# Kernel tuning notes

Measured on AMD Instinct MI355X. Metric: run time of the kernel, lower is better.

The kernel has to match this reference:

```python
import jax, jax.numpy as jnp
import numpy as np

N_NODES = 50000
N_EDGES = 800000
D_IN, D_HID, D_OUT = 128, 128, 256
EPS = 1e-12  # F.normalize eps


def _mean_aggr(h, src, dst, n):
    # scatter-mean of source features onto destination nodes
    msg_sum = jax.ops.segment_sum(h[src], dst, num_segments=n)
    deg = jax.ops.segment_sum(jnp.ones((src.shape[0],), h.dtype), dst, num_segments=n)
    return msg_sum / jnp.maximum(deg, 1.0)[:, None]


def _l2_normalize(h):
    # F.normalize(p=2, dim=1): divide by clamped L2 norm
    nrm = jnp.sqrt(jnp.sum(h * h, axis=1, keepdims=True))
    return h / jnp.maximum(nrm, EPS)


def setup_inputs() -> dict:
    key = jax.random.key(0)
    ks = jax.random.split(key, 8)
    x = jax.random.normal(ks[0], (N_NODES, D_IN), dtype=jnp.float32)
    edge_index = jax.random.randint(ks[1], (2, N_EDGES), 0, N_NODES, dtype=jnp.int64 if jax.config.read('jax_enable_x64') else jnp.int32)
    s = 1.0 / np.sqrt(D_IN)
    W1_l = jax.random.uniform(ks[2], (D_IN, D_HID), jnp.float32, -s, s)
    W1_r = jax.random.uniform(ks[3], (D_IN, D_HID), jnp.float32, -s, s)
    b1 = jnp.zeros((D_HID,), jnp.float32)
    s2 = 1.0 / np.sqrt(D_HID)
    W2_l = jax.random.uniform(ks[4], (D_HID, D_OUT), jnp.float32, -s2, s2)
    W2_r = jax.random.uniform(ks[5], (D_HID, D_OUT), jnp.float32, -s2, s2)
    b2 = jnp.zeros((D_OUT,), jnp.float32)
    return {"x": x, "edge_index": edge_index, "W1_l": W1_l, "W1_r": W1_r,
            "b1": b1, "W2_l": W2_l, "W2_r": W2_r, "b2": b2}


def reference(x, edge_index, W1_l, W1_r, b1, W2_l, W2_r, b2):
    src, dst = edge_index[0], edge_index[1]
    n = x.shape[0]
    # SAGEConv 1: lin_l(mean_aggr(x)) + lin_r(x) + bias
    h = _mean_aggr(x, src, dst, n) @ W1_l + x @ W1_r + b1
    # dropout is identity in eval mode
    h = _l2_normalize(jax.nn.sigmoid(h))
    # SAGEConv 2
    h = _mean_aggr(h, src, dst, n) @ W2_l + h @ W2_r + b2
    h = _l2_normalize(jax.nn.sigmoid(h))
    return jax.nn.log_softmax(h, axis=-1)
```

## Files before the change

### kernel.cpp

```cpp
#include <hip/hip_runtime.h>

#define NN 50000
#define NE 800000
#define NB 782
#define CAP 1536


__device__ __forceinline__ unsigned short f2bf(float f) {
    union { float f; unsigned u; } v; v.f = f;
    unsigned u = v.u;
    return (unsigned short)((u + 0x7fffu + ((u >> 16) & 1u)) >> 16);
}
__device__ __forceinline__ float bfu_lo(unsigned p) {
    union { unsigned u; float f; } v; v.u = p << 16; return v.f;
}
__device__ __forceinline__ float bfu_hi(unsigned p) {
    union { unsigned u; float f; } v; v.u = p & 0xffff0000u; return v.f;
}

typedef __bf16 bf16x8 __attribute__((ext_vector_type(8)));
typedef float f32x4 __attribute__((ext_vector_type(4)));
typedef unsigned uint4v __attribute__((ext_vector_type(4)));
union U16 { uint4 u; bf16x8 v; };
union U16v { uint4v q; bf16x8 v; };


__global__ __launch_bounds__(512) void binscatter_kernel(const int* __restrict__ src,
                                                         const int* __restrict__ dst,
                                                         int* __restrict__ bcnt,
                                                         unsigned* __restrict__ ebuf) {
    __shared__ int hist[NB];
    __shared__ int base[NB];
    const int BE = 8192;
    int tid = threadIdx.x;
    int e0 = blockIdx.x * BE;
    for (int i = tid; i < NB; i += 512) hist[i] = 0;
    __syncthreads();
    for (int i = tid; i < BE; i += 512) {
        int e = e0 + i;
        if (e < NE) atomicAdd(&hist[dst[e] >> 6], 1);
    }
    __syncthreads();
    for (int i = tid; i < NB; i += 512) {
        int c = hist[i];
        base[i] = c ? atomicAdd(&bcnt[i], c) : 0;
        hist[i] = 0;
    }
    __syncthreads();
    for (int i = tid; i < BE; i += 512) {
        int e = e0 + i;
        if (e < NE) {
            int d = dst[e], b = d >> 6;
            int slot = base[b] + atomicAdd(&hist[b], 1);
            if (slot < CAP)
                ebuf[(size_t)b * CAP + slot] = (unsigned)src[e] | ((unsigned)(d & 63) << 16);
        }
    }
}

__global__ __launch_bounds__(256) void csr_kernel(const int* __restrict__ bcnt,
                                                  const unsigned* __restrict__ ebuf,
                                                  int* __restrict__ rowptr,
                                                  int* __restrict__ col) {
    __shared__ int red[256];
    __shared__ int deg[64];
    __shared__ int cur[64];
    __shared__ int cbase_s;
    int b = blockIdx.x, tid = threadIdx.x;
    int s = 0;
    for (int i = tid; i < b; i += 256) s += bcnt[i];
    red[tid] = s;
    if (tid < 64) deg[tid] = 0;
    __syncthreads();
    for (int off = 128; off; off >>= 1) {
        if (tid < off) red[tid] += red[tid + off];
        __syncthreads();
    }
    if (tid == 0) cbase_s = red[0];
    __syncthreads();
    int cnt = bcnt[b], cbase = cbase_s;
    if (cnt > CAP) cnt = CAP;
    const unsigned* eb = ebuf + (size_t)b * CAP;
    for (int i = tid; i < cnt; i += 256) atomicAdd(&deg[(eb[i] >> 16) & 63], 1);
    __syncthreads();
    if (tid == 0) {
        int run = 0;
        for (int j = 0; j < 64; j++) { cur[j] = run; run += deg[j]; }
    }
    __syncthreads();
    int node = b * 64 + tid;
    if (tid < 64 && node < NN) rowptr[node] = cbase + cur[tid];
    if (b == NB - 1 && tid == 0) rowptr[NN] = NE;
    __syncthreads();
    for (int i = tid; i < cnt; i += 256) {
        unsigned e = eb[i];
        int pos = atomicAdd(&cur[(e >> 16) & 63], 1);
        col[cbase + pos] = (int)(e & 0xffffu);
    }
}


template <int N>
__device__ __forceinline__ void pack_one(const float* __restrict__ Wl,
                                         const float* __restrict__ Wr,
                                         unsigned short* __restrict__ Wp, int t) {
    int lane = t & 63, c = t >> 6;
    int ks = c & 7, nt = c >> 3;
    int n = nt * 16 + (lane & 15);
    int kq = ks * 32 + (lane >> 4) * 8;
    unsigned short tmp[8];
#pragma unroll
    for (int j = 0; j < 8; j++) {
        int k = kq + j;
        float w = (k < 128) ? Wl[(size_t)k * N + n] : Wr[(size_t)(k - 128) * N + n];
        tmp[j] = f2bf(w);
    }
    ((ushort4*)Wp)[(size_t)c * 128 + lane * 2 + 0] = make_ushort4(tmp[0], tmp[1], tmp[2], tmp[3]);
    ((ushort4*)Wp)[(size_t)c * 128 + lane * 2 + 1] = make_ushort4(tmp[4], tmp[5], tmp[6], tmp[7]);
}

#define CAST_BLK (NN * 128 / 4 / 256)

__global__ void castpack_kernel(const float* __restrict__ in, unsigned short* __restrict__ outp,
                                const float* __restrict__ W1l, const float* __restrict__ W1r,
                                unsigned short* __restrict__ W1p,
                                const float* __restrict__ W2l, const float* __restrict__ W2r,
                                unsigned short* __restrict__ W2p) {
    if (blockIdx.x < CAST_BLK) {
        int i = blockIdx.x * 256 + threadIdx.x;
        float4 f = ((const float4*)in)[i];
        ushort4 o;
        o.x = f2bf(f.x); o.y = f2bf(f.y); o.z = f2bf(f.z); o.w = f2bf(f.w);
        ((ushort4*)outp)[i] = o;
    } else {
        int t = (blockIdx.x - CAST_BLK) * 256 + threadIdx.x;
        if (t < 8 * 8 * 64) pack_one<128>(W1l, W1r, W1p, t);
        else if (t < 8 * 8 * 64 + 16 * 8 * 64) pack_one<256>(W2l, W2r, W2p, t - 8 * 8 * 64);
    }
}


__global__ void aggregate_bf_kernel(const int* __restrict__ rowptr, const int* __restrict__ col,
                                    const uint4* __restrict__ feat4,
                                    uint4* __restrict__ out4) {
    int wid = (blockIdx.x * blockDim.x + threadIdx.x) >> 6;
    int lane = threadIdx.x & 63;
    if (wid >= NN) return;
    int beg = rowptr[wid], end = rowptr[wid + 1];
    int deg = end - beg;
    int g = lane >> 4, c16 = lane & 15;
    int nmain = deg < 64 ? deg : 64;
    int cidx = (lane < nmain) ? col[beg + lane] : 0;
    float acc[8];
#pragma unroll
    for (int j = 0; j < 8; j++) acc[j] = 0.f;
    for (int i = 0; i < nmain; i += 16) {
        int e0 = i + g, e1 = i + 4 + g, e2 = i + 8 + g, e3 = i + 12 + g;
        int s0 = __shfl(cidx, e0);
        int s1 = __shfl(cidx, e1);
        int s2 = __shfl(cidx, e2);
        int s3 = __shfl(cidx, e3);
        uint4 v0 = make_uint4(0u, 0u, 0u, 0u);
        uint4 v1 = make_uint4(0u, 0u, 0u, 0u);
        uint4 v2 = make_uint4(0u, 0u, 0u, 0u);
        uint4 v3 = make_uint4(0u, 0u, 0u, 0u);
        if (e0 < nmain) v0 = feat4[(size_t)s0 * 16 + c16];
        if (e1 < nmain) v1 = feat4[(size_t)s1 * 16 + c16];
        if (e2 < nmain) v2 = feat4[(size_t)s2 * 16 + c16];
        if (e3 < nmain) v3 = feat4[(size_t)s3 * 16 + c16];
        acc[0] += bfu_lo(v0.x); acc[1] += bfu_hi(v0.x);
        acc[2] += bfu_lo(v0.y); acc[3] += bfu_hi(v0.y);
        acc[4] += bfu_lo(v0.z); acc[5] += bfu_hi(v0.z);
        acc[6] += bfu_lo(v0.w); acc[7] += bfu_hi(v0.w);
        acc[0] += bfu_lo(v1.x); acc[1] += bfu_hi(v1.x);
        acc[2] += bfu_lo(v1.y); acc[3] += bfu_hi(v1.y);
        acc[4] += bfu_lo(v1.z); acc[5] += bfu_hi(v1.z);
        acc[6] += bfu_lo(v1.w); acc[7] += bfu_hi(v1.w);
        acc[0] += bfu_lo(v2.x); acc[1] += bfu_hi(v2.x);
        acc[2] += bfu_lo(v2.y); acc[3] += bfu_hi(v2.y);
        acc[4] += bfu_lo(v2.z); acc[5] += bfu_hi(v2.z);
        acc[6] += bfu_lo(v2.w); acc[7] += bfu_hi(v2.w);
        acc[0] += bfu_lo(v3.x); acc[1] += bfu_hi(v3.x);
        acc[2] += bfu_lo(v3.y); acc[3] += bfu_hi(v3.y);
        acc[4] += bfu_lo(v3.z); acc[5] += bfu_hi(v3.z);
        acc[6] += bfu_lo(v3.w); acc[7] += bfu_hi(v3.w);
    }
    for (int i = 64; i < deg; i += 4) {
        int idx = beg + i + g;
        if (idx < end) {
            int s = col[idx];
            uint4 v = feat4[(size_t)s * 16 + c16];
            acc[0] += bfu_lo(v.x); acc[1] += bfu_hi(v.x);
            acc[2] += bfu_lo(v.y); acc[3] += bfu_hi(v.y);
            acc[4] += bfu_lo(v.z); acc[5] += bfu_hi(v.z);
            acc[6] += bfu_lo(v.w); acc[7] += bfu_hi(v.w);
        }
    }
#pragma unroll
    for (int j = 0; j < 8; j++) {
        acc[j] += __shfl_xor(acc[j], 16);
        acc[j] += __shfl_xor(acc[j], 32);
    }
    if (g == 0) {
        float inv = (deg > 0) ? 1.0f / (float)deg : 0.0f;
        uint4 o;
        o.x = (unsigned)f2bf(acc[0] * inv) | ((unsigned)f2bf(acc[1] * inv) << 16);
        o.y = (unsigned)f2bf(acc[2] * inv) | ((unsigned)f2bf(acc[3] * inv) << 16);
        o.z = (unsigned)f2bf(acc[4] * inv) | ((unsigned)f2bf(acc[5] * inv) << 16);
        o.w = (unsigned)f2bf(acc[6] * inv) | ((unsigned)f2bf(acc[7] * inv) << 16);
        out4[(size_t)wid * 16 + c16] = o;
    }
}


template <int N, bool FINAL>
__global__ __launch_bounds__(512, 2) void gemm_mfma_kernel(
    const unsigned short* __restrict__ A0, const unsigned short* __restrict__ A1,
    const unsigned short* __restrict__ Wp, const float* __restrict__ bias,
    void* __restrict__ outp, int M) {
    const int NT = N / 32;
    __shared__ float redS[2][64];
    __shared__ float redE[2][64];
    int tid = threadIdx.x, wave = tid >> 6, lane = tid & 63;
    int half = wave & 1;
    int rg = wave >> 1;
    int quad = lane >> 4, col = lane & 15;
    int m_base = blockIdx.x * 64 + rg * 16;
    int row = m_base + col;
    int row_ld = row < M ? row : M - 1;

    bf16x8 a[8];
    const uint4* a0p = (const uint4*)(A0 + (size_t)row_ld * 128 + quad * 8);
    const uint4* a1p = (const uint4*)(A1 + (size_t)row_ld * 128 + quad * 8);
#pragma unroll
    for (int ks = 0; ks < 4; ks++) { U16 u; u.u = a0p[ks * 4]; a[ks] = u.v; }
#pragma unroll
    for (int ks = 0; ks < 4; ks++) { U16 u; u.u = a1p[ks * 4]; a[4 + ks] = u.v; }

    f32x4 acc[NT];
#pragma unroll
    for (int nt = 0; nt < NT; nt++) acc[nt] = (f32x4){0.f, 0.f, 0.f, 0.f};

    const uint4* wp = (const uint4*)Wp;
#pragma unroll
    for (int ks = 0; ks < 8; ks++) {
        uint4v w[NT];
#pragma unroll
        for (int j = 0; j < NT; j++) {
            const uint4* ap = wp + ((size_t)((half * NT + j) * 8 + ks) * 64 + lane);
            asm volatile("global_load_dwordx4 %0, %1, off" : "=&v"(w[j]) : "v"(ap));
        }
        asm volatile("s_waitcnt vmcnt(0)" ::: "memory");
        __builtin_amdgcn_sched_barrier(0);
#pragma unroll
        for (int j = 0; j < NT; j++) {
            U16v u; u.q = w[j];
            acc[j] = __builtin_amdgcn_mfma_f32_16x16x32_bf16(a[ks], u.v, acc[j], 0, 0, 0);
        }
    }

    int rbase = rg * 16 + quad * 4;

    float ssq[4] = {0.f, 0.f, 0.f, 0.f};
#pragma unroll
    for (int nt = 0; nt < NT; nt++) {
        float bv = bias[half * (NT * 16) + nt * 16 + col];
#pragma unroll
        for (int r = 0; r < 4; r++) {
            float z = acc[nt][r] + bv;
            float s = 1.0f / (1.0f + __expf(-z));
            acc[nt][r] = s;
            ssq[r] += s * s;
        }
    }
#pragma unroll
    for (int r = 0; r < 4; r++) {
#pragma unroll
        for (int off = 1; off < 16; off <<= 1) ssq[r] += __shfl_xor(ssq[r], off, 16);
    }
    if (col == 0) {
#pragma unroll
        for (int r = 0; r < 4; r++) redS[half][rbase + r] = ssq[r];
    }
    __syncthreads();
#pragma unroll
    for (int r = 0; r < 4; r++) {
        float tot = redS[0][rbase + r] + redS[1][rbase + r];
        float sc = 1.0f / fmaxf(sqrtf(tot), 1e-12f);
#pragma unroll
        for (int nt = 0; nt < NT; nt++) acc[nt][r] *= sc;
    }

    if (FINAL) {
        float se[4];
#pragma unroll
        for (int r = 0; r < 4; r++) {
            se[r] = 0.f;
#pragma unroll
            for (int nt = 0; nt < NT; nt++) se[r] += __expf(acc[nt][r]);
#pragma unroll
            for (int off = 1; off < 16; off <<= 1) se[r] += __shfl_xor(se[r], off, 16);
        }
        if (col == 0) {
#pragma unroll
            for (int r = 0; r < 4; r++) redE[half][rbase + r] = se[r];
        }
        __syncthreads();
        float* op = (float*)outp;
#pragma unroll
        for (int r = 0; r < 4; r++) {
            float lse = __logf(redE[0][rbase + r] + redE[1][rbase + r]);
            int m = m_base + quad * 4 + r;
            if (m < M) {
#pragma unroll
                for (int nt = 0; nt < NT; nt++)
                    op[(size_t)m * N + half * (NT * 16) + nt * 16 + col] = acc[nt][r] - lse;
            }
        }
    } else {
        unsigned short* op = (unsigned short*)outp;
#pragma unroll
        for (int r = 0; r < 4; r++) {
            int m = m_base + quad * 4 + r;
            if (m < M) {
#pragma unroll
                for (int nt = 0; nt < NT; nt++)
                    op[(size_t)m * N + half * (NT * 16) + nt * 16 + col] = f2bf(acc[nt][r]);
            }
        }
    }
}


extern "C" void kernel_launch(void* const* d_in, const int* in_sizes, int n_in,
                              void* d_out, int out_size, void* d_ws, size_t ws_size,
                              hipStream_t stream) {
    const float* x   = (const float*)d_in[0];
    const int*   ei  = (const int*)d_in[1];
    const float* W1l = (const float*)d_in[2];
    const float* W1r = (const float*)d_in[3];
    const float* b1  = (const float*)d_in[4];
    const float* W2l = (const float*)d_in[5];
    const float* W2r = (const float*)d_in[6];
    const float* b2  = (const float*)d_in[7];
    float* out = (float*)d_out;

    const int* src = ei;
    const int* dst = ei + NE;

    char* ws = (char*)d_ws;
    size_t off = 0;
    auto alloc = [&](size_t bytes) -> void* {
        void* p = ws + off;
        off += (bytes + 255) / 256 * 256;
        return p;
    };
    int* rowptr     = (int*)alloc((size_t)(NN + 1) * 4);
    int* col        = (int*)alloc((size_t)NE * 4);
    int* bcnt       = (int*)alloc((size_t)NB * 4);
    unsigned* ebuf  = (unsigned*)alloc((size_t)NB * CAP * 4);
    unsigned short* x_bf   = (unsigned short*)alloc((size_t)NN * 128 * 2);
    unsigned short* agg_bf = (unsigned short*)alloc((size_t)NN * 128 * 2);
    unsigned short* h1_bf  = (unsigned short*)alloc((size_t)NN * 128 * 2);
    unsigned short* W1p    = (unsigned short*)alloc((size_t)8 * 8 * 64 * 8 * 2);
    unsigned short* W2p    = (unsigned short*)alloc((size_t)16 * 8 * 64 * 8 * 2);

    hipMemsetAsync(bcnt, 0, (size_t)NB * 4, stream);
    binscatter_kernel<<<(NE + 8191) / 8192, 512, 0, stream>>>(src, dst, bcnt, ebuf);
    csr_kernel<<<NB, 256, 0, stream>>>(bcnt, ebuf, rowptr, col);

    castpack_kernel<<<CAST_BLK + 48, 256, 0, stream>>>(x, x_bf, W1l, W1r, W1p, W2l, W2r, W2p);

    aggregate_bf_kernel<<<(NN + 3) / 4, 256, 0, stream>>>(rowptr, col, (const uint4*)x_bf,
                                                          (uint4*)agg_bf);
    gemm_mfma_kernel<128, false><<<(NN + 63) / 64, 512, 0, stream>>>(agg_bf, x_bf, W1p, b1,
                                                                     h1_bf, NN);
    aggregate_bf_kernel<<<(NN + 3) / 4, 256, 0, stream>>>(rowptr, col, (const uint4*)h1_bf,
                                                          (uint4*)agg_bf);
    gemm_mfma_kernel<256, true><<<(NN + 63) / 64, 512, 0, stream>>>(agg_bf, h1_bf, W2p, b2,
                                                                    out, NN);
}
```

Before: 232.1 us.

## Fuse neighbor mean aggregation into the MFMA layer GEMM kernel via shared memory

The separate aggregation kernel is merged into the GEMM kernel. Each 512-thread block first gathers and averages neighbor features for its 64 rows into a padded LDS tile, then runs the MFMA GEMM reading the aggregated operand from LDS. This removes the agg_bf global write and re-read plus two kernel launches per forward pass. In exchange, the gather phase runs with only the GEMM kernel's occupancy (launch bounds 512,2), each wave walks 8 nodes serially, and a block barrier is added, which may hide gather latency less well than the standalone aggregation kernel did.

After: 242.3 us. 4.4% more time.

```diff
diff --git a/kernel.cpp b/kernel.cpp
--- a/kernel.cpp
+++ b/kernel.cpp
@@ -140,100 +140,103 @@
 }
 
 
-__global__ void aggregate_bf_kernel(const int* __restrict__ rowptr, const int* __restrict__ col,
-                                    const uint4* __restrict__ feat4,
-                                    uint4* __restrict__ out4) {
-    int wid = (blockIdx.x * blockDim.x + threadIdx.x) >> 6;
-    int lane = threadIdx.x & 63;
-    if (wid >= NN) return;
-    int beg = rowptr[wid], end = rowptr[wid + 1];
-    int deg = end - beg;
-    int g = lane >> 4, c16 = lane & 15;
-    int nmain = deg < 64 ? deg : 64;
-    int cidx = (lane < nmain) ? col[beg + lane] : 0;
-    float acc[8];
-#pragma unroll
-    for (int j = 0; j < 8; j++) acc[j] = 0.f;
-    for (int i = 0; i < nmain; i += 16) {
-        int e0 = i + g, e1 = i + 4 + g, e2 = i + 8 + g, e3 = i + 12 + g;
-        int s0 = __shfl(cidx, e0);
-        int s1 = __shfl(cidx, e1);
-        int s2 = __shfl(cidx, e2);
-        int s3 = __shfl(cidx, e3);
-        uint4 v0 = make_uint4(0u, 0u, 0u, 0u);
-        uint4 v1 = make_uint4(0u, 0u, 0u, 0u);
-        uint4 v2 = make_uint4(0u, 0u, 0u, 0u);
-        uint4 v3 = make_uint4(0u, 0u, 0u, 0u);
-        if (e0 < nmain) v0 = feat4[(size_t)s0 * 16 + c16];
-        if (e1 < nmain) v1 = feat4[(size_t)s1 * 16 + c16];
-        if (e2 < nmain) v2 = feat4[(size_t)s2 * 16 + c16];
-        if (e3 < nmain) v3 = feat4[(size_t)s3 * 16 + c16];
-        acc[0] += bfu_lo(v0.x); acc[1] += bfu_hi(v0.x);
-        acc[2] += bfu_lo(v0.y); acc[3] += bfu_hi(v0.y);
-        acc[4] += bfu_lo(v0.z); acc[5] += bfu_hi(v0.z);
-        acc[6] += bfu_lo(v0.w); acc[7] += bfu_hi(v0.w);
-        acc[0] += bfu_lo(v1.x); acc[1] += bfu_hi(v1.x);
-        acc[2] += bfu_lo(v1.y); acc[3] += bfu_hi(v1.y);
-        acc[4] += bfu_lo(v1.z); acc[5] += bfu_hi(v1.z);
-        acc[6] += bfu_lo(v1.w); acc[7] += bfu_hi(v1.w);
-        acc[0] += bfu_lo(v2.x); acc[1] += bfu_hi(v2.x);
-        acc[2] += bfu_lo(v2.y); acc[3] += bfu_hi(v2.y);
-        acc[4] += bfu_lo(v2.z); acc[5] += bfu_hi(v2.z);
-        acc[6] += bfu_lo(v2.w); acc[7] += bfu_hi(v2.w);
-        acc[0] += bfu_lo(v3.x); acc[1] += bfu_hi(v3.x);
-        acc[2] += bfu_lo(v3.y); acc[3] += bfu_hi(v3.y);
-        acc[4] += bfu_lo(v3.z); acc[5] += bfu_hi(v3.z);
-        acc[6] += bfu_lo(v3.w); acc[7] += bfu_hi(v3.w);
-    }
-    for (int i = 64; i < deg; i += 4) {
-        int idx = beg + i + g;
-        if (idx < end) {
-            int s = col[idx];
-            uint4 v = feat4[(size_t)s * 16 + c16];
-            acc[0] += bfu_lo(v.x); acc[1] += bfu_hi(v.x);
-            acc[2] += bfu_lo(v.y); acc[3] += bfu_hi(v.y);
-            acc[4] += bfu_lo(v.z); acc[5] += bfu_hi(v.z);
-            acc[6] += bfu_lo(v.w); acc[7] += bfu_hi(v.w);
-        }
-    }
-#pragma unroll
-    for (int j = 0; j < 8; j++) {
-        acc[j] += __shfl_xor(acc[j], 16);
-        acc[j] += __shfl_xor(acc[j], 32);
-    }
-    if (g == 0) {
-        float inv = (deg > 0) ? 1.0f / (float)deg : 0.0f;
-        uint4 o;
-        o.x = (unsigned)f2bf(acc[0] * inv) | ((unsigned)f2bf(acc[1] * inv) << 16);
-        o.y = (unsigned)f2bf(acc[2] * inv) | ((unsigned)f2bf(acc[3] * inv) << 16);
-        o.z = (unsigned)f2bf(acc[4] * inv) | ((unsigned)f2bf(acc[5] * inv) << 16);
-        o.w = (unsigned)f2bf(acc[6] * inv) | ((unsigned)f2bf(acc[7] * inv) << 16);
-        out4[(size_t)wid * 16 + c16] = o;
-    }
-}
-
-
 template <int N, bool FINAL>
-__global__ __launch_bounds__(512, 2) void gemm_mfma_kernel(
-    const unsigned short* __restrict__ A0, const unsigned short* __restrict__ A1,
+__global__ __launch_bounds__(512, 2) void layer_kernel(
+    const unsigned short* __restrict__ feat,
+    const int* __restrict__ rowptr, const int* __restrict__ cols,
     const unsigned short* __restrict__ Wp, const float* __restrict__ bias,
     void* __restrict__ outp, int M) {
     const int NT = N / 32;
+    __shared__ __align__(16) unsigned short sA[64][136];
     __shared__ float redS[2][64];
     __shared__ float redE[2][64];
     int tid = threadIdx.x, wave = tid >> 6, lane = tid & 63;
+    int g = lane >> 4, c16 = lane & 15;
+    const uint4* feat4 = (const uint4*)feat;
+
+    for (int j = 0; j < 8; j++) {
+        int node = blockIdx.x * 64 + wave * 8 + j;
+        int node_ld = node < NN ? node : NN - 1;
+        int beg = rowptr[node_ld], end = rowptr[node_ld + 1];
+        int deg = end - beg;
+        int nmain = deg < 64 ? deg : 64;
+        int cidx = (lane < nmain) ? cols[beg + lane] : 0;
+        float acc[8];
+#pragma unroll
+        for (int q = 0; q < 8; q++) acc[q] = 0.f;
+        for (int i = 0; i < nmain; i += 16) {
+            int e0 = i + g, e1 = i + 4 + g, e2 = i + 8 + g, e3 = i + 12 + g;
+            int s0 = __shfl(cidx, e0);
+            int s1 = __shfl(cidx, e1);
+            int s2 = __shfl(cidx, e2);
+            int s3 = __shfl(cidx, e3);
+            uint4 v0 = make_uint4(0u, 0u, 0u, 0u);
+            uint4 v1 = make_uint4(0u, 0u, 0u, 0u);
+            uint4 v2 = make_uint4(0u, 0u, 0u, 0u);
+            uint4 v3 = make_uint4(0u, 0u, 0u, 0u);
+            if (e0 < nmain) v0 = feat4[(size_t)s0 * 16 + c16];
+            if (e1 < nmain) v1 = feat4[(size_t)s1 * 16 + c16];
+            if (e2 < nmain) v2 = feat4[(size_t)s2 * 16 + c16];
+            if (e3 < nmain) v3 = feat4[(size_t)s3 * 16 + c16];
+            acc[0] += bfu_lo(v0.x); acc[1] += bfu_hi(v0.x);
+            acc[2] += bfu_lo(v0.y); acc[3] += bfu_hi(v0.y);
+            acc[4] += bfu_lo(v0.z); acc[5] += bfu_hi(v0.z);
+            acc[6] += bfu_lo(v0.w); acc[7] += bfu_hi(v0.w);
+            acc[0] += bfu_lo(v1.x); acc[1] += bfu_hi(v1.x);
+            acc[2] += bfu_lo(v1.y); acc[3] += bfu_hi(v1.y);
+            acc[4] += bfu_lo(v1.z); acc[5] += bfu_hi(v1.z);
+            acc[6] += bfu_lo(v1.w); acc[7] += bfu_hi(v1.w);
+            acc[0] += bfu_lo(v2.x); acc[1] += bfu_hi(v2.x);
+            acc[2] += bfu_lo(v2.y); acc[3] += bfu_hi(v2.y);
+            acc[4] += bfu_lo(v2.z); acc[5] += bfu_hi(v2.z);
+            acc[6] += bfu_lo(v2.w); acc[7] += bfu_hi(v2.w);
+            acc[0] += bfu_lo(v3.x); acc[1] += bfu_hi(v3.x);
+            acc[2] += bfu_lo(v3.y); acc[3] += bfu_hi(v3.y);
+            acc[4] += bfu_lo(v3.z); acc[5] += bfu_hi(v3.z);
+            acc[6] += bfu_lo(v3.w); acc[7] += bfu_hi(v3.w);
+        }
+        for (int i = 64; i < deg; i += 4) {
+            int idx = beg + i + g;
+            if (idx < end) {
+                int s = cols[idx];
+                uint4 v = feat4[(size_t)s * 16 + c16];
+                acc[0] += bfu_lo(v.x); acc[1] += bfu_hi(v.x);
+                acc[2] += bfu_lo(v.y); acc[3] += bfu_hi(v.y);
+                acc[4] += bfu_lo(v.z); acc[5] += bfu_hi(v.z);
+                acc[6] += bfu_lo(v.w); acc[7] += bfu_hi(v.w);
+            }
+        }
+#pragma unroll
+        for (int q = 0; q < 8; q++) {
+            acc[q] += __shfl_xor(acc[q], 16);
+            acc[q] += __shfl_xor(acc[q], 32);
+        }
+        if (g == 0) {
+            float inv = (deg > 0) ? 1.0f / (float)deg : 0.0f;
+            uint4 o;
+            o.x = (unsigned)f2bf(acc[0] * inv) | ((unsigned)f2bf(acc[1] * inv) << 16);
+            o.y = (unsigned)f2bf(acc[2] * inv) | ((unsigned)f2bf(acc[3] * inv) << 16);
+            o.z = (unsigned)f2bf(acc[4] * inv) | ((unsigned)f2bf(acc[5] * inv) << 16);
+            o.w = (unsigned)f2bf(acc[6] * inv) | ((unsigned)f2bf(acc[7] * inv) << 16);
+            *(uint4*)&sA[wave * 8 + j][c16 * 8] = o;
+        }
+    }
+    __syncthreads();
+
     int half = wave & 1;
     int rg = wave >> 1;
-    int quad = lane >> 4, col = lane & 15;
+    int quad = g, colx = c16;
     int m_base = blockIdx.x * 64 + rg * 16;
-    int row = m_base + col;
+    int row = m_base + colx;
     int row_ld = row < M ? row : M - 1;
 
     bf16x8 a[8];
-    const uint4* a0p = (const uint4*)(A0 + (size_t)row_ld * 128 + quad * 8);
-    const uint4* a1p = (const uint4*)(A1 + (size_t)row_ld * 128 + quad * 8);
-#pragma unroll
-    for (int ks = 0; ks < 4; ks++) { U16 u; u.u = a0p[ks * 4]; a[ks] = u.v; }
+#pragma unroll
+    for (int ks = 0; ks < 4; ks++) {
+        U16 u; u.u = *(const uint4*)&sA[rg * 16 + colx][quad * 8 + ks * 32];
+        a[ks] = u.v;
+    }
+    const uint4* a1p = (const uint4*)(feat + (size_t)row_ld * 128 + quad * 8);
 #pragma unroll
     for (int ks = 0; ks < 4; ks++) { U16 u; u.u = a1p[ks * 4]; a[4 + ks] = u.v; }
 
@@ -264,7 +267,7 @@
     float ssq[4] = {0.f, 0.f, 0.f, 0.f};
 #pragma unroll
     for (int nt = 0; nt < NT; nt++) {
-        float bv = bias[half * (NT * 16) + nt * 16 + col];
+        float bv = bias[half * (NT * 16) + nt * 16 + colx];
 #pragma unroll
         for (int r = 0; r < 4; r++) {
             float z = acc[nt][r] + bv;
@@ -278,7 +281,7 @@
 #pragma unroll
         for (int off = 1; off < 16; off <<= 1) ssq[r] += __shfl_xor(ssq[r], off, 16);
     }
-    if (col == 0) {
+    if (colx == 0) {
 #pragma unroll
         for (int r = 0; r < 4; r++) redS[half][rbase + r] = ssq[r];
     }
@@ -301,7 +304,7 @@
 #pragma unroll
             for (int off = 1; off < 16; off <<= 1) se[r] += __shfl_xor(se[r], off, 16);
         }
-        if (col == 0) {
+        if (colx == 0) {
 #pragma unroll
             for (int r = 0; r < 4; r++) redE[half][rbase + r] = se[r];
         }
@@ -314,7 +317,7 @@
             if (m < M) {
 #pragma unroll
                 for (int nt = 0; nt < NT; nt++)
-                    op[(size_t)m * N + half * (NT * 16) + nt * 16 + col] = acc[nt][r] - lse;
+                    op[(size_t)m * N + half * (NT * 16) + nt * 16 + colx] = acc[nt][r] - lse;
             }
         }
     } else {
@@ -325,7 +328,7 @@
             if (m < M) {
 #pragma unroll
                 for (int nt = 0; nt < NT; nt++)
-                    op[(size_t)m * N + half * (NT * 16) + nt * 16 + col] = f2bf(acc[nt][r]);
+                    op[(size_t)m * N + half * (NT * 16) + nt * 16 + colx] = f2bf(acc[nt][r]);
             }
         }
     }
@@ -360,7 +363,6 @@
     int* bcnt       = (int*)alloc((size_t)NB * 4);
     unsigned* ebuf  = (unsigned*)alloc((size_t)NB * CAP * 4);
     unsigned short* x_bf   = (unsigned short*)alloc((size_t)NN * 128 * 2);
-    unsigned short* agg_bf = (unsigned short*)alloc((size_t)NN * 128 * 2);
     unsigned short* h1_bf  = (unsigned short*)alloc((size_t)NN * 128 * 2);
     unsigned short* W1p    = (unsigned short*)alloc((size_t)8 * 8 * 64 * 8 * 2);
     unsigned short* W2p    = (unsigned short*)alloc((size_t)16 * 8 * 64 * 8 * 2);
@@ -371,12 +373,8 @@
 
     castpack_kernel<<<CAST_BLK + 48, 256, 0, stream>>>(x, x_bf, W1l, W1r, W1p, W2l, W2r, W2p);
 
-    aggregate_bf_kernel<<<(NN + 3) / 4, 256, 0, stream>>>(rowptr, col, (const uint4*)x_bf,
-                                                          (uint4*)agg_bf);
-    gemm_mfma_kernel<128, false><<<(NN + 63) / 64, 512, 0, stream>>>(agg_bf, x_bf, W1p, b1,
-                                                                     h1_bf, NN);
-    aggregate_bf_kernel<<<(NN + 3) / 4, 256, 0, stream>>>(rowptr, col, (const uint4*)h1_bf,
-                                                          (uint4*)agg_bf);
-    gemm_mfma_kernel<256, true><<<(NN + 63) / 64, 512, 0, stream>>>(agg_bf, h1_bf, W2p, b2,
-                                                                    out, NN);
-}
+    layer_kernel<128, false><<<(NN + 63) / 64, 512, 0, stream>>>(x_bf, rowptr, col, W1p, b1,
+                                                                 h1_bf, NN);
+    layer_kernel<256, true><<<(NN + 63) / 64, 512, 0, stream>>>(h1_bf, rowptr, col, W2p, b2,
+                                                                out, NN);
+}
```
